# Performance work log

Measured on AMD Instinct MI355X. Metric: run time of the kernel, lower is better.

## Reference

```python
import jax, jax.numpy as jnp
import numpy as np

N = 50000
E = 1600000
D_IN = 128
D_HID = 64
BN_EPS = 1e-5


def setup_inputs() -> dict:
    key = jax.random.key(0)
    ks = jax.random.split(key, 12)
    x = jax.random.normal(ks[0], (N, D_IN), dtype=jnp.float32)
    edge_index_sc = jax.random.randint(ks[1], (2, E), 0, N, dtype=jnp.int64)
    edge_weight_sc = jax.random.uniform(ks[2], (E,), dtype=jnp.float32)
    edge_index_fc = jax.random.randint(ks[3], (2, E), 0, N, dtype=jnp.int64)
    edge_weight_fc = jax.random.uniform(ks[4], (E,), dtype=jnp.float32)
    # learned parameters
    alpha = jnp.float32(0.5)
    W1 = jax.random.normal(ks[5], (D_IN, D_HID), dtype=jnp.float32) / np.sqrt(D_IN)
    b1 = jnp.zeros((D_HID,), dtype=jnp.float32)
    W2 = jax.random.normal(ks[6], (D_HID, D_HID), dtype=jnp.float32) / np.sqrt(D_HID)
    b2 = jnp.zeros((D_HID,), dtype=jnp.float32)
    gamma1 = jnp.ones((D_HID,), dtype=jnp.float32)
    beta1 = jnp.zeros((D_HID,), dtype=jnp.float32)
    gamma2 = jnp.ones((D_HID,), dtype=jnp.float32)
    beta2 = jnp.zeros((D_HID,), dtype=jnp.float32)
    return {"x": x, "edge_index_sc": edge_index_sc, "edge_weight_sc": edge_weight_sc,
            "edge_index_fc": edge_index_fc, "edge_weight_fc": edge_weight_fc,
            "alpha": alpha, "W1": W1, "b1": b1, "W2": W2, "b2": b2,
            "gamma1": gamma1, "beta1": beta1, "gamma2": gamma2, "beta2": beta2}


def _gcn_layer(h, W, b, src, dst, norm, n):
    # h: [N, d_in] -> [N, d_out]; PyG GCNConv: transform, then weighted scatter-add
    h = h @ W
    msg = h[src] * norm[:, None]                # [E+N, d_out] gather + scale
    out = jax.ops.segment_sum(msg, dst, num_segments=n)
    return out + b


def _bn_relu(h, gamma, beta):
    # BatchNorm1d (training-mode batch stats, biased variance) + ReLU
    mean = jnp.mean(h, axis=0)
    var = jnp.var(h, axis=0)
    h = (h - mean) * jax.lax.rsqrt(var + BN_EPS) * gamma + beta
    return jax.nn.relu(h)


def reference(x, edge_index_sc, edge_weight_sc, edge_index_fc, edge_weight_fc,
              alpha, W1, b1, W2, b2, gamma1, beta1, gamma2, beta2):
    n = x.shape[0]
    a = jax.nn.sigmoid(alpha)
    # mixed weights on SC topology (edge_index_fc unused, as in original)
    w_mix = a * edge_weight_sc + (1.0 - a) * edge_weight_fc
    # add self loops (weight 1) and compute symmetric GCN normalization
    loop = jnp.arange(n, dtype=edge_index_sc.dtype)
    src = jnp.concatenate([edge_index_sc[0], loop])
    dst = jnp.concatenate([edge_index_sc[1], loop])
    w = jnp.concatenate([w_mix, jnp.ones((n,), dtype=w_mix.dtype)])
    deg = jax.ops.segment_sum(w, dst, num_segments=n)
    dinv = jnp.where(deg > 0, jax.lax.rsqrt(jnp.maximum(deg, 1e-12)), 0.0)
    norm = dinv[src] * w * dinv[dst]
    h = _gcn_layer(x, W1, b1, src, dst, norm, n)
    h = _bn_relu(h, gamma1, beta1)
    h = _gcn_layer(h, W2, b2, src, dst, norm, n)
    h = _bn_relu(h, gamma2, beta2)
    return h  # dropout is identity in eval mode
```

## Files before the change

### kernel.cpp

```cpp
#include <hip/hip_runtime.h>
#include <hip/hip_fp16.h>
#include <math.h>

#define N_NODES 50000
#define N_EDGES 1600000
#define D_INF   128
#define D_HID   64
#define BN_EPS  1e-5f
#define NBINS   391
#define BINCAP  4608
#define EPB     6250
#define GEMM1B  3125
#define NPAIR   3125
#define NCOPY   64

struct SmGemm { float sw[D_INF * D_HID]; float sx[16 * D_INF]; };
struct SmBin  { int hcnt[NBINS]; int hbase[NBINS]; };
union SmPre { SmGemm g; SmBin a; };

__global__ __launch_bounds__(256) void k_pre(const float* __restrict__ wsc,
                                             const float* __restrict__ wfc,
                                             const int*   __restrict__ ei,
                                             const float* __restrict__ alpha,
                                             int* __restrict__ bin_cur,
                                             unsigned long long* __restrict__ binned,
                                             const float* __restrict__ x,
                                             const float* __restrict__ W,
                                             __half* __restrict__ ha,
                                             __half* __restrict__ hb) {
    __shared__ SmPre sm;
    int t = threadIdx.x;
    if (blockIdx.x < 256) {
        int e0 = blockIdx.x * EPB;
        for (int b = t; b < NBINS; b += 256) sm.a.hcnt[b] = 0;
        __syncthreads();
        for (int i = t; i < EPB; i += 256)
            atomicAdd(&sm.a.hcnt[ei[N_EDGES + e0 + i] >> 7], 1);
        __syncthreads();
        for (int b = t; b < NBINS; b += 256) {
            int c = sm.a.hcnt[b];
            sm.a.hbase[b] = c ? atomicAdd(&bin_cur[b], c) : 0;
            sm.a.hcnt[b] = 0;
        }
        __syncthreads();
        float a = 1.0f / (1.0f + expf(-alpha[0]));
        for (int i = t; i < EPB; i += 256) {
            int e = e0 + i;
            int s = ei[e], d = ei[N_EDGES + e];
            float wm = fmaf(a, wsc[e] - wfc[e], wfc[e]);
            int bin = d >> 7;
            int slot = atomicAdd(&sm.a.hcnt[bin], 1);
            int gpos = sm.a.hbase[bin] + slot;
            if (gpos < BINCAP) {
                unsigned long long ent =
                    ((unsigned long long)__float_as_uint(wm) << 32)
                    | (unsigned int)(s | ((d & 127) << 16));
                binned[(size_t)bin * BINCAP + gpos] = ent;
            }
        }
    } else {
        int row0 = (blockIdx.x - 256) * 16;
#pragma unroll
        for (int j = 0; j < 32; ++j) sm.g.sw[t + j * 256] = W[t + j * 256];
#pragma unroll
        for (int j = 0; j < 8; ++j) {
            int i = t + j * 256;
            int r = i >> 7, k = i & 127;
            sm.g.sx[i] = x[(row0 + r) * D_INF + k];
        }
        __syncthreads();
        int c = t & 63, rg = (t >> 6) * 4;
        float a0 = 0, a1 = 0, a2 = 0, a3 = 0;
#pragma unroll 4
        for (int k = 0; k < D_INF; ++k) {
            float w = sm.g.sw[k * D_HID + c];
            a0 = fmaf(sm.g.sx[(rg + 0) * D_INF + k], w, a0);
            a1 = fmaf(sm.g.sx[(rg + 1) * D_INF + k], w, a1);
            a2 = fmaf(sm.g.sx[(rg + 2) * D_INF + k], w, a2);
            a3 = fmaf(sm.g.sx[(rg + 3) * D_INF + k], w, a3);
        }
        __half* tbl = (c < 32) ? ha : hb;
        int cc = c & 31;
        tbl[(row0 + rg + 0) * 32 + cc] = __float2half_rn(a0);
        tbl[(row0 + rg + 1) * 32 + cc] = __float2half_rn(a1);
        tbl[(row0 + rg + 2) * 32 + cc] = __float2half_rn(a2);
        tbl[(row0 + rg + 3) * 32 + cc] = __float2half_rn(a3);
    }
}

__global__ __launch_bounds__(512) void k_binB(const int* __restrict__ bin_cur,
                                              const unsigned long long* __restrict__ binned,
                                              int2*  __restrict__ row_se,
                                              float* __restrict__ dinv,
                                              __half* __restrict__ ha,
                                              __half* __restrict__ hb,
                                              unsigned int* __restrict__ csr) {
    __shared__ unsigned long long stage[BINCAP];
    __shared__ int   ncnt[128];
    __shared__ float ndeg[128];
    __shared__ int   sscan[128];
    __shared__ float sdinv[128];
    __shared__ int   lb[128];
    int t = threadIdx.x;
    int bin = blockIdx.x;
    if (t < 128) { ncnt[t] = 0; ndeg[t] = 0.0f; }
    int cnt = min(bin_cur[bin], BINCAP);
    const unsigned long long* mybin = binned + (size_t)bin * BINCAP;
    for (int i = t; i < cnt; i += 512) stage[i] = mybin[i];
    __syncthreads();
    for (int i = t; i < cnt; i += 512) {
        unsigned long long ent = stage[i];
        unsigned int lo = (unsigned int)ent;
        int nl = (lo >> 16) & 127;
        float wm = __uint_as_float((unsigned int)(ent >> 32));
        atomicAdd(&ncnt[nl], 1);
        atomicAdd(&ndeg[nl], wm);
    }
    __syncthreads();
    int node0 = bin << 7;
    int nnodes = min(128, N_NODES - node0);
    if (t < 128) {
        float dv = rsqrtf(1.0f + ndeg[t]);
        sdinv[t] = dv;
        if (t < nnodes) dinv[node0 + t] = dv;
        sscan[t] = ncnt[t];
    }
    __syncthreads();
    for (int off = 1; off < 128; off <<= 1) {
        int u = (t >= off && t < 128) ? sscan[t - off] : 0;
        __syncthreads();
        if (t < 128) sscan[t] += u;
        __syncthreads();
    }
    if (t < nnodes) {
        int s = bin * BINCAP + sscan[t] - ncnt[t];
        row_se[node0 + t] = make_int2(s, s + ncnt[t]);
        lb[t] = s;
    }
    __syncthreads();
    int nh = nnodes * 32;
    for (int i = t; i < nh; i += 512) {
        int n = i >> 5, c = i & 31;
        float dv = sdinv[n];
        int idx = (node0 + n) * 32 + c;
        ha[idx] = __float2half_rn(__half2float(ha[idx]) * dv);
        hb[idx] = __float2half_rn(__half2float(hb[idx]) * dv);
    }
    if (t < 128) ncnt[t] = 0;
    __syncthreads();
    for (int i = t; i < cnt; i += 512) {
        unsigned long long ent = stage[i];
        unsigned int lo = (unsigned int)ent;
        int nl  = (lo >> 16) & 127;
        int src = lo & 0xFFFFu;
        float wm = __uint_as_float((unsigned int)(ent >> 32));
        int slot = atomicAdd(&ncnt[nl], 1);
        unsigned short wh = __half_as_ushort(__float2half_rn(wm));
        csr[lb[nl] + slot] = (unsigned int)src | ((unsigned int)wh << 16);
    }
}

__device__ inline float hdec(unsigned int u) {
    return __half2float(__ushort_as_half((unsigned short)(u >> 16)));
}

__global__ __launch_bounds__(512) void k_gather(const __half* __restrict__ ha,
                                                const __half* __restrict__ hb,
                                                const unsigned int* __restrict__ csr,
                                                const int2*  __restrict__ row_se,
                                                const float* __restrict__ dinv,
                                                const float* __restrict__ bias,
                                                float* __restrict__ out,
                                                float* __restrict__ stat) {
    __shared__ float s1[512], s2[512];
    int t = threadIdx.x;
    int half = blockIdx.x & 1;
    const float4* __restrict__ h4 = (const float4*)(half ? hb : ha);
    int node = (blockIdx.x >> 1) * 16 + (t >> 5);
    int ln = t & 31;
    int sg = ln >> 2;
    int cq = ln & 3;
    int2 se = row_se[node];
    float dd = dinv[node];
    float acc[8];
    if (sg == 0) {
        float4 sv = h4[node * 4 + cq];
        const __half2* p = reinterpret_cast<const __half2*>(&sv);
#pragma unroll
        for (int i = 0; i < 4; ++i) {
            float2 f = __half22float2(p[i]);
            acc[2 * i] = f.x; acc[2 * i + 1] = f.y;
        }
    } else {
#pragma unroll
        for (int i = 0; i < 8; ++i) acc[i] = 0.0f;
    }
    for (int b = se.x; b < se.y; b += 32) {
        int c0 = min(32, se.y - b);
        int cm = c0 - 1;
        unsigned int my = (ln < c0) ? csr[b + ln] : 0u;
        unsigned int u0 = __shfl(my, min(sg,      cm), 32);
        unsigned int u1 = __shfl(my, min(sg + 8,  cm), 32);
        unsigned int u2 = __shfl(my, min(sg + 16, cm), 32);
        unsigned int u3 = __shfl(my, min(sg + 24, cm), 32);
        float4 r0 = h4[(u0 & 0xFFFFu) * 4 + cq];
        float4 r1 = h4[(u1 & 0xFFFFu) * 4 + cq];
        float4 r2 = h4[(u2 & 0xFFFFu) * 4 + cq];
        float4 r3 = h4[(u3 & 0xFFFFu) * 4 + cq];
        float w0 = (sg      < c0) ? hdec(u0) : 0.0f;
        float w1 = (sg + 8  < c0) ? hdec(u1) : 0.0f;
        float w2 = (sg + 16 < c0) ? hdec(u2) : 0.0f;
        float w3 = (sg + 24 < c0) ? hdec(u3) : 0.0f;
        const __half2* p0 = reinterpret_cast<const __half2*>(&r0);
        const __half2* p1 = reinterpret_cast<const __half2*>(&r1);
        const __half2* p2 = reinterpret_cast<const __half2*>(&r2);
        const __half2* p3 = reinterpret_cast<const __half2*>(&r3);
#pragma unroll
        for (int i = 0; i < 4; ++i) {
            float2 f0 = __half22float2(p0[i]);
            float2 f1 = __half22float2(p1[i]);
            float2 f2 = __half22float2(p2[i]);
            float2 f3 = __half22float2(p3[i]);
            acc[2*i]   = fmaf(f0.x, w0, acc[2*i]);
            acc[2*i+1] = fmaf(f0.y, w0, acc[2*i+1]);
            acc[2*i]   = fmaf(f1.x, w1, acc[2*i]);
            acc[2*i+1] = fmaf(f1.y, w1, acc[2*i+1]);
            acc[2*i]   = fmaf(f2.x, w2, acc[2*i]);
            acc[2*i+1] = fmaf(f2.y, w2, acc[2*i+1]);
            acc[2*i]   = fmaf(f3.x, w3, acc[2*i]);
            acc[2*i+1] = fmaf(f3.y, w3, acc[2*i+1]);
        }
    }
#pragma unroll
    for (int off = 16; off >= 4; off >>= 1) {
#pragma unroll
        for (int i = 0; i < 8; ++i) acc[i] += __shfl_down(acc[i], off, 32);
    }
    if (ln < 4) {
        int col0 = half * 32 + cq * 8;
        float v[8];
#pragma unroll
        for (int i = 0; i < 8; ++i) v[i] = fmaf(acc[i], dd, bias[col0 + i]);
        float4* o = (float4*)out;
        o[node * 16 + half * 8 + cq * 2]     = make_float4(v[0], v[1], v[2], v[3]);
        o[node * 16 + half * 8 + cq * 2 + 1] = make_float4(v[4], v[5], v[6], v[7]);
        int lb = (t >> 5) * 32 + cq * 8;
#pragma unroll
        for (int i = 0; i < 8; ++i) { s1[lb + i] = v[i]; s2[lb + i] = v[i] * v[i]; }
    }
    __syncthreads();
#pragma unroll
    for (int off = 256; off >= 32; off >>= 1) {
        if (t < off) { s1[t] += s1[t + off]; s2[t] += s2[t + off]; }
        __syncthreads();
    }
    if (t < 32) {
        int cp = (blockIdx.x >> 1) & (NCOPY - 1);
        int col = half * 32 + t;
        atomicAdd(&stat[cp * 128 + col],      s1[t]);
        atomicAdd(&stat[cp * 128 + 64 + col], s2[t]);
    }
}

__global__ __launch_bounds__(256) void k_gemm2_bn(const float* __restrict__ hin,
                                                  const float* __restrict__ stat,
                                                  const float* __restrict__ gamma,
                                                  const float* __restrict__ beta,
                                                  const float* __restrict__ W,
                                                  const float* __restrict__ dinv,
                                                  __half* __restrict__ ha,
                                                  __half* __restrict__ hb) {
    __shared__ float sw[D_HID * D_HID];
    __shared__ float sx[16 * D_HID];
    __shared__ float sc[D_HID], sh[D_HID];
    int t = threadIdx.x;
    int row0 = blockIdx.x * 16;
#pragma unroll
    for (int j = 0; j < 16; ++j) sw[t + j * 256] = W[t + j * 256];
    if (t < 64) {
        float s = 0.0f, q = 0.0f;
#pragma unroll 8
        for (int c = 0; c < NCOPY; ++c) {
            s += stat[c * 128 + t];
            q += stat[c * 128 + 64 + t];
        }
        const float invn = 1.0f / (float)N_NODES;
        float mean = s * invn;
        float var  = q * invn - mean * mean;
        float g    = gamma[t] * rsqrtf(var + BN_EPS);
        sc[t] = g;
        sh[t] = beta[t] - mean * g;
    }
    __syncthreads();
#pragma unroll
    for (int j = 0; j < 4; ++j) {
        int i = t + j * 256;
        int k = i & 63;
        sx[i] = fmaxf(0.0f, fmaf(hin[row0 * D_HID + i], sc[k], sh[k]));
    }
    __syncthreads();
    int c = t & 63, rg = (t >> 6) * 4;
    float a0 = 0, a1 = 0, a2 = 0, a3 = 0;
#pragma unroll 4
    for (int k = 0; k < D_HID; ++k) {
        float w = sw[k * D_HID + c];
        a0 = fmaf(sx[(rg + 0) * D_HID + k], w, a0);
        a1 = fmaf(sx[(rg + 1) * D_HID + k], w, a1);
        a2 = fmaf(sx[(rg + 2) * D_HID + k], w, a2);
        a3 = fmaf(sx[(rg + 3) * D_HID + k], w, a3);
    }
    __half* tbl = (c < 32) ? ha : hb;
    int cc = c & 31;
    tbl[(row0 + rg + 0) * 32 + cc] = __float2half_rn(a0 * dinv[row0 + rg + 0]);
    tbl[(row0 + rg + 1) * 32 + cc] = __float2half_rn(a1 * dinv[row0 + rg + 1]);
    tbl[(row0 + rg + 2) * 32 + cc] = __float2half_rn(a2 * dinv[row0 + rg + 2]);
    tbl[(row0 + rg + 3) * 32 + cc] = __float2half_rn(a3 * dinv[row0 + rg + 3]);
}

__global__ __launch_bounds__(256) void k_bn_apply_relu(float4* __restrict__ h,
                                                       const float* __restrict__ stat,
                                                       const float* __restrict__ gamma,
                                                       const float* __restrict__ beta) {
    __shared__ float sc[D_HID], sh[D_HID];
    int t = threadIdx.x;
    if (t < 64) {
        float s = 0.0f, q = 0.0f;
#pragma unroll 8
        for (int c = 0; c < NCOPY; ++c) {
            s += stat[c * 128 + t];
            q += stat[c * 128 + 64 + t];
        }
        const float invn = 1.0f / (float)N_NODES;
        float mean = s * invn;
        float var  = q * invn - mean * mean;
        float g    = gamma[t] * rsqrtf(var + BN_EPS);
        sc[t] = g;
        sh[t] = beta[t] - mean * g;
    }
    __syncthreads();
    int idx = blockIdx.x * 256 + t;
    if (idx >= N_NODES * D_HID / 4) return;
    int j = (idx & 15) * 4;
    float4 v = h[idx];
    v.x = fmaxf(0.0f, fmaf(v.x, sc[j],     sh[j]));
    v.y = fmaxf(0.0f, fmaf(v.y, sc[j + 1], sh[j + 1]));
    v.z = fmaxf(0.0f, fmaf(v.z, sc[j + 2], sh[j + 2]));
    v.w = fmaxf(0.0f, fmaf(v.w, sc[j + 3], sh[j + 3]));
    h[idx] = v;
}

extern "C" void kernel_launch(void* const* d_in, const int* in_sizes, int n_in,
                              void* d_out, int out_size, void* d_ws, size_t ws_size,
                              hipStream_t stream) {
    const float* x     = (const float*)d_in[0];
    const int*   ei_sc = (const int*)  d_in[1];
    const float* w_sc  = (const float*)d_in[2];
    const float* w_fc  = (const float*)d_in[4];
    const float* alpha = (const float*)d_in[5];
    const float* W1    = (const float*)d_in[6];
    const float* b1    = (const float*)d_in[7];
    const float* W2    = (const float*)d_in[8];
    const float* b2    = (const float*)d_in[9];
    const float* g1    = (const float*)d_in[10];
    const float* be1   = (const float*)d_in[11];
    const float* g2    = (const float*)d_in[12];
    const float* be2   = (const float*)d_in[13];
    float* out = (float*)d_out;

    unsigned long long* binned = (unsigned long long*)d_ws;
    int2*  row_se  = (int2*)(binned + (size_t)NBINS * BINCAP);
    int*   bin_cur = (int*)(row_se + N_NODES);
    float* stats   = (float*)(bin_cur + 400);
    float* dinv    = stats + 2 * NCOPY * 128;
    unsigned int* csr = (unsigned int*)(dinv + N_NODES);
    __half* ha     = (__half*)(csr + (size_t)NBINS * BINCAP);
    __half* hb     = ha + (size_t)N_NODES * 32;
    float* agg     = (float*)(hb + (size_t)N_NODES * 32);

    const int gV4 = (N_NODES * D_HID / 4 + 255) / 256;
    const int gGA = NPAIR * 2;
    const int gGM = N_NODES / 16;

    hipMemsetAsync(bin_cur, 0, (400 + 2 * NCOPY * 128) * sizeof(int), stream);
    k_pre <<<256 + GEMM1B, 256, 0, stream>>>(w_sc, w_fc, ei_sc, alpha,
                                             bin_cur, binned, x, W1, ha, hb);
    k_binB<<<NBINS, 512, 0, stream>>>(bin_cur, binned, row_se, dinv, ha, hb, csr);

    k_gather  <<<gGA, 512, 0, stream>>>(ha, hb, csr, row_se, dinv, b1, agg, stats);

    k_gemm2_bn<<<gGM, 256, 0, stream>>>(agg, stats, g1, be1, W2, dinv, ha, hb);
    k_gather  <<<gGA, 512, 0, stream>>>(ha, hb, csr, row_se, dinv, b2, out,
                                        stats + NCOPY * 128);
    k_bn_apply_relu<<<gV4, 256, 0, stream>>>((float4*)out, stats + NCOPY * 128,
                                             g2, be2);
}
```

Before: 284.8 us.

## Fuse post-binning stages into one persistent cooperative kernel with grid syncs

```diff
diff --git a/kernel.cpp b/kernel.cpp
--- a/kernel.cpp
+++ b/kernel.cpp
@@ -1,4 +1,5 @@
 #include <hip/hip_runtime.h>
+#include <hip/hip_cooperative_groups.h>
 #include <hip/hip_fp16.h>
 #include <math.h>
 
@@ -88,95 +89,91 @@
     }
 }
 
-__global__ __launch_bounds__(512) void k_binB(const int* __restrict__ bin_cur,
-                                              const unsigned long long* __restrict__ binned,
-                                              int2*  __restrict__ row_se,
-                                              float* __restrict__ dinv,
-                                              __half* __restrict__ ha,
-                                              __half* __restrict__ hb,
-                                              unsigned int* __restrict__ csr) {
-    __shared__ unsigned long long stage[BINCAP];
-    __shared__ int   ncnt[128];
-    __shared__ float ndeg[128];
-    __shared__ int   sscan[128];
-    __shared__ float sdinv[128];
-    __shared__ int   lb[128];
-    int t = threadIdx.x;
-    int bin = blockIdx.x;
-    if (t < 128) { ncnt[t] = 0; ndeg[t] = 0.0f; }
+struct SmBinB {
+    unsigned long long stage[BINCAP];
+    int   ncnt[128];
+    float ndeg[128];
+    int   sscan[128];
+    float sdinv[128];
+    int   lb[128];
+};
+struct SmGath { float s1[512]; float s2[512]; };
+struct SmG2   { float sw[D_HID * D_HID]; float sx[16 * D_HID];
+                float sc[D_HID]; float sh[D_HID]; };
+union SmMega { SmBinB b; SmGath s; SmG2 g; };
+
+__device__ __forceinline__ void binB_body(int bin, int t, SmBinB& s,
+        const int* bin_cur, const unsigned long long* binned,
+        int2* row_se, float* dinv, __half* ha, __half* hb, unsigned int* csr) {
+    if (t < 128) { s.ncnt[t] = 0; s.ndeg[t] = 0.0f; }
     int cnt = min(bin_cur[bin], BINCAP);
     const unsigned long long* mybin = binned + (size_t)bin * BINCAP;
-    for (int i = t; i < cnt; i += 512) stage[i] = mybin[i];
+    for (int i = t; i < cnt; i += 512) s.stage[i] = mybin[i];
     __syncthreads();
     for (int i = t; i < cnt; i += 512) {
-        unsigned long long ent = stage[i];
+        unsigned long long ent = s.stage[i];
         unsigned int lo = (unsigned int)ent;
         int nl = (lo >> 16) & 127;
         float wm = __uint_as_float((unsigned int)(ent >> 32));
-        atomicAdd(&ncnt[nl], 1);
-        atomicAdd(&ndeg[nl], wm);
+        atomicAdd(&s.ncnt[nl], 1);
+        atomicAdd(&s.ndeg[nl], wm);
     }
     __syncthreads();
     int node0 = bin << 7;
     int nnodes = min(128, N_NODES - node0);
     if (t < 128) {
-        float dv = rsqrtf(1.0f + ndeg[t]);
-        sdinv[t] = dv;
+        float dv = rsqrtf(1.0f + s.ndeg[t]);
+        s.sdinv[t] = dv;
         if (t < nnodes) dinv[node0 + t] = dv;
-        sscan[t] = ncnt[t];
+        s.sscan[t] = s.ncnt[t];
     }
     __syncthreads();
     for (int off = 1; off < 128; off <<= 1) {
-        int u = (t >= off && t < 128) ? sscan[t - off] : 0;
-        __syncthreads();
-        if (t < 128) sscan[t] += u;
+        int u = (t >= off && t < 128) ? s.sscan[t - off] : 0;
+        __syncthreads();
+        if (t < 128) s.sscan[t] += u;
         __syncthreads();
     }
     if (t < nnodes) {
-        int s = bin * BINCAP + sscan[t] - ncnt[t];
-        row_se[node0 + t] = make_int2(s, s + ncnt[t]);
-        lb[t] = s;
+        int st = bin * BINCAP + s.sscan[t] - s.ncnt[t];
+        row_se[node0 + t] = make_int2(st, st + s.ncnt[t]);
+        s.lb[t] = st;
     }
     __syncthreads();
     int nh = nnodes * 32;
     for (int i = t; i < nh; i += 512) {
         int n = i >> 5, c = i & 31;
-        float dv = sdinv[n];
+        float dv = s.sdinv[n];
         int idx = (node0 + n) * 32 + c;
         ha[idx] = __float2half_rn(__half2float(ha[idx]) * dv);
         hb[idx] = __float2half_rn(__half2float(hb[idx]) * dv);
     }
-    if (t < 128) ncnt[t] = 0;
+    if (t < 128) s.ncnt[t] = 0;
     __syncthreads();
     for (int i = t; i < cnt; i += 512) {
-        unsigned long long ent = stage[i];
+        unsigned long long ent = s.stage[i];
         unsigned int lo = (unsigned int)ent;
         int nl  = (lo >> 16) & 127;
         int src = lo & 0xFFFFu;
         float wm = __uint_as_float((unsigned int)(ent >> 32));
-        int slot = atomicAdd(&ncnt[nl], 1);
+        int slot = atomicAdd(&s.ncnt[nl], 1);
         unsigned short wh = __half_as_ushort(__float2half_rn(wm));
-        csr[lb[nl] + slot] = (unsigned int)src | ((unsigned int)wh << 16);
-    }
+        csr[s.lb[nl] + slot] = (unsigned int)src | ((unsigned int)wh << 16);
+    }
+    __syncthreads();
 }
 
 __device__ inline float hdec(unsigned int u) {
     return __half2float(__ushort_as_half((unsigned short)(u >> 16)));
 }
 
-__global__ __launch_bounds__(512) void k_gather(const __half* __restrict__ ha,
-                                                const __half* __restrict__ hb,
-                                                const unsigned int* __restrict__ csr,
-                                                const int2*  __restrict__ row_se,
-                                                const float* __restrict__ dinv,
-                                                const float* __restrict__ bias,
-                                                float* __restrict__ out,
-                                                float* __restrict__ stat) {
-    __shared__ float s1[512], s2[512];
-    int t = threadIdx.x;
-    int half = blockIdx.x & 1;
-    const float4* __restrict__ h4 = (const float4*)(half ? hb : ha);
-    int node = (blockIdx.x >> 1) * 16 + (t >> 5);
+__device__ __forceinline__ void gather_body(int vb, int t, SmGath& sm,
+        const __half* ha, const __half* hb, const unsigned int* csr,
+        const int2* row_se, const float* dinv, const float* bias,
+        float* out, float* stat) {
+    int half = vb & 1;
+    const float4* h4 = (const float4*)(half ? hb : ha);
+    int node = (vb >> 1) * 16 + (t >> 5);
     int ln = t & 31;
     int sg = ln >> 2;
     int cq = ln & 3;
@@ -246,37 +243,25 @@
         o[node * 16 + half * 8 + cq * 2 + 1] = make_float4(v[4], v[5], v[6], v[7]);
         int lb = (t >> 5) * 32 + cq * 8;
 #pragma unroll
-        for (int i = 0; i < 8; ++i) { s1[lb + i] = v[i]; s2[lb + i] = v[i] * v[i]; }
+        for (int i = 0; i < 8; ++i) { sm.s1[lb + i] = v[i]; sm.s2[lb + i] = v[i] * v[i]; }
     }
     __syncthreads();
 #pragma unroll
     for (int off = 256; off >= 32; off >>= 1) {
-        if (t < off) { s1[t] += s1[t + off]; s2[t] += s2[t + off]; }
+        if (t < off) { sm.s1[t] += sm.s1[t + off]; sm.s2[t] += sm.s2[t + off]; }
         __syncthreads();
     }
     if (t < 32) {
-        int cp = (blockIdx.x >> 1) & (NCOPY - 1);
+        int cp = (vb >> 1) & (NCOPY - 1);
         int col = half * 32 + t;
-        atomicAdd(&stat[cp * 128 + col],      s1[t]);
-        atomicAdd(&stat[cp * 128 + 64 + col], s2[t]);
-    }
-}
-
-__global__ __launch_bounds__(256) void k_gemm2_bn(const float* __restrict__ hin,
-                                                  const float* __restrict__ stat,
-                                                  const float* __restrict__ gamma,
-                                                  const float* __restrict__ beta,
-                                                  const float* __restrict__ W,
-                                                  const float* __restrict__ dinv,
-                                                  __half* __restrict__ ha,
-                                                  __half* __restrict__ hb) {
-    __shared__ float sw[D_HID * D_HID];
-    __shared__ float sx[16 * D_HID];
-    __shared__ float sc[D_HID], sh[D_HID];
-    int t = threadIdx.x;
-    int row0 = blockIdx.x * 16;
-#pragma unroll
-    for (int j = 0; j < 16; ++j) sw[t + j * 256] = W[t + j * 256];
+        atomicAdd(&stat[cp * 128 + col],      sm.s1[t]);
+        atomicAdd(&stat[cp * 128 + 64 + col], sm.s2[t]);
+    }
+    __syncthreads();
+}
+
+__device__ __forceinline__ void bn_coef(int t, float* sc, float* sh,
+        const float* stat, const float* gamma, const float* beta) {
     if (t < 64) {
         float s = 0.0f, q = 0.0f;
 #pragma unroll 8
@@ -291,62 +276,118 @@
         sc[t] = g;
         sh[t] = beta[t] - mean * g;
     }
-    __syncthreads();
-#pragma unroll
-    for (int j = 0; j < 4; ++j) {
-        int i = t + j * 256;
+}
+
+__device__ __forceinline__ void gemm2_sub(int row0, int t, SmG2& g,
+        const float* hin, const float* dinv, __half* ha, __half* hb) {
+#pragma unroll
+    for (int j = 0; j < 2; ++j) {
+        int i = t + j * 512;
         int k = i & 63;
-        sx[i] = fmaxf(0.0f, fmaf(hin[row0 * D_HID + i], sc[k], sh[k]));
-    }
-    __syncthreads();
-    int c = t & 63, rg = (t >> 6) * 4;
-    float a0 = 0, a1 = 0, a2 = 0, a3 = 0;
+        g.sx[i] = fmaxf(0.0f, fmaf(hin[row0 * D_HID + i], g.sc[k], g.sh[k]));
+    }
+    __syncthreads();
+    int c = t & 63, r2 = (t >> 6) * 2;
+    float a0 = 0, a1 = 0;
 #pragma unroll 4
     for (int k = 0; k < D_HID; ++k) {
-        float w = sw[k * D_HID + c];
-        a0 = fmaf(sx[(rg + 0) * D_HID + k], w, a0);
-        a1 = fmaf(sx[(rg + 1) * D_HID + k], w, a1);
-        a2 = fmaf(sx[(rg + 2) * D_HID + k], w, a2);
-        a3 = fmaf(sx[(rg + 3) * D_HID + k], w, a3);
+        float w = g.sw[k * D_HID + c];
+        a0 = fmaf(g.sx[(r2 + 0) * D_HID + k], w, a0);
+        a1 = fmaf(g.sx[(r2 + 1) * D_HID + k], w, a1);
     }
     __half* tbl = (c < 32) ? ha : hb;
     int cc = c & 31;
-    tbl[(row0 + rg + 0) * 32 + cc] = __float2half_rn(a0 * dinv[row0 + rg + 0]);
-    tbl[(row0 + rg + 1) * 32 + cc] = __float2half_rn(a1 * dinv[row0 + rg + 1]);
-    tbl[(row0 + rg + 2) * 32 + cc] = __float2half_rn(a2 * dinv[row0 + rg + 2]);
-    tbl[(row0 + rg + 3) * 32 + cc] = __float2half_rn(a3 * dinv[row0 + rg + 3]);
-}
-
-__global__ __launch_bounds__(256) void k_bn_apply_relu(float4* __restrict__ h,
-                                                       const float* __restrict__ stat,
-                                                       const float* __restrict__ gamma,
-                                                       const float* __restrict__ beta) {
+    tbl[(row0 + r2 + 0) * 32 + cc] = __float2half_rn(a0 * dinv[row0 + r2 + 0]);
+    tbl[(row0 + r2 + 1) * 32 + cc] = __float2half_rn(a1 * dinv[row0 + r2 + 1]);
+    __syncthreads();
+}
+
+__global__ __launch_bounds__(512, 6) void k_mega(
+        const int* bin_cur, const unsigned long long* binned,
+        int2* row_se, float* dinv, __half* ha, __half* hb, unsigned int* csr,
+        float* agg, float* stats, const float* b1,
+        const float* g1, const float* be1, const float* W2,
+        const float* b2, float* out, const float* g2, const float* be2) {
+    __shared__ SmMega sm;
+    int t = threadIdx.x;
+    int nb = gridDim.x;
+    cooperative_groups::grid_group gg = cooperative_groups::this_grid();
+
+    for (int i = blockIdx.x * 512 + t; i < 2 * NCOPY * 128; i += nb * 512)
+        stats[i] = 0.0f;
+    for (int bin = blockIdx.x; bin < NBINS; bin += nb)
+        binB_body(bin, t, sm.b, bin_cur, binned, row_se, dinv, ha, hb, csr);
+    gg.sync();
+
+    for (int vb = blockIdx.x; vb < NPAIR * 2; vb += nb)
+        gather_body(vb, t, sm.s, ha, hb, csr, row_se, dinv, b1, agg, stats);
+    gg.sync();
+
+    bn_coef(t, sm.g.sc, sm.g.sh, stats, g1, be1);
+#pragma unroll
+    for (int j = 0; j < 8; ++j) sm.g.sw[t + j * 512] = W2[t + j * 512];
+    __syncthreads();
+    for (int vb = blockIdx.x; vb < N_NODES / 16; vb += nb)
+        gemm2_sub(vb * 16, t, sm.g, agg, dinv, ha, hb);
+    gg.sync();
+
+    for (int vb = blockIdx.x; vb < NPAIR * 2; vb += nb)
+        gather_body(vb, t, sm.s, ha, hb, csr, row_se, dinv, b2, out,
+                    stats + NCOPY * 128);
+    gg.sync();
+
+    bn_coef(t, sm.g.sc, sm.g.sh, stats + NCOPY * 128, g2, be2);
+    __syncthreads();
+    float4* o4 = (float4*)out;
+    for (int i = blockIdx.x * 512 + t; i < N_NODES * 16; i += nb * 512) {
+        int j = (i & 15) * 4;
+        float4 v = o4[i];
+        v.x = fmaxf(0.0f, fmaf(v.x, sm.g.sc[j],     sm.g.sh[j]));
+        v.y = fmaxf(0.0f, fmaf(v.y, sm.g.sc[j + 1], sm.g.sh[j + 1]));
+        v.z = fmaxf(0.0f, fmaf(v.z, sm.g.sc[j + 2], sm.g.sh[j + 2]));
+        v.w = fmaxf(0.0f, fmaf(v.w, sm.g.sc[j + 3], sm.g.sh[j + 3]));
+        o4[i] = v;
+    }
+}
+
+__global__ __launch_bounds__(512) void k_binB_w(const int* bin_cur,
+        const unsigned long long* binned, int2* row_se, float* dinv,
+        __half* ha, __half* hb, unsigned int* csr) {
+    __shared__ SmBinB s;
+    binB_body(blockIdx.x, threadIdx.x, s, bin_cur, binned, row_se, dinv, ha, hb, csr);
+}
+__global__ __launch_bounds__(512) void k_gath_w(const __half* ha, const __half* hb,
+        const unsigned int* csr, const int2* row_se, const float* dinv,
+        const float* bias, float* out, float* stat) {
+    __shared__ SmGath s;
+    gather_body(blockIdx.x, threadIdx.x, s, ha, hb, csr, row_se, dinv, bias, out, stat);
+}
+__global__ __launch_bounds__(512) void k_g2_w(const float* hin, const float* stat,
+        const float* gamma, const float* beta, const float* W,
+        const float* dinv, __half* ha, __half* hb) {
+    __shared__ SmG2 g;
+    int t = threadIdx.x;
+    bn_coef(t, g.sc, g.sh, stat, gamma, beta);
+#pragma unroll
+    for (int j = 0; j < 8; ++j) g.sw[t + j * 512] = W[t + j * 512];
+    __syncthreads();
+    gemm2_sub(blockIdx.x * 16, t, g, hin, dinv, ha, hb);
+}
+__global__ __launch_bounds__(512) void k_bnap_w(float4* h, const float* stat,
+        const float* gamma, const float* beta) {
     __shared__ float sc[D_HID], sh[D_HID];
     int t = threadIdx.x;
-    if (t < 64) {
-        float s = 0.0f, q = 0.0f;
-#pragma unroll 8
-        for (int c = 0; c < NCOPY; ++c) {
-            s += stat[c * 128 + t];
-            q += stat[c * 128 + 64 + t];
-        }
-        const float invn = 1.0f / (float)N_NODES;
-        float mean = s * invn;
-        float var  = q * invn - mean * mean;
-        float g    = gamma[t] * rsqrtf(var + BN_EPS);
-        sc[t] = g;
-        sh[t] = beta[t] - mean * g;
-    }
-    __syncthreads();
-    int idx = blockIdx.x * 256 + t;
-    if (idx >= N_NODES * D_HID / 4) return;
-    int j = (idx & 15) * 4;
-    float4 v = h[idx];
-    v.x = fmaxf(0.0f, fmaf(v.x, sc[j],     sh[j]));
-    v.y = fmaxf(0.0f, fmaf(v.y, sc[j + 1], sh[j + 1]));
-    v.z = fmaxf(0.0f, fmaf(v.z, sc[j + 2], sh[j + 2]));
-    v.w = fmaxf(0.0f, fmaf(v.w, sc[j + 3], sh[j + 3]));
-    h[idx] = v;
+    bn_coef(t, sc, sh, stat, gamma, beta);
+    __syncthreads();
+    for (int i = blockIdx.x * 512 + t; i < N_NODES * 16; i += gridDim.x * 512) {
+        int j = (i & 15) * 4;
+        float4 v = h[i];
+        v.x = fmaxf(0.0f, fmaf(v.x, sc[j],     sh[j]));
+        v.y = fmaxf(0.0f, fmaf(v.y, sc[j + 1], sh[j + 1]));
+        v.z = fmaxf(0.0f, fmaf(v.z, sc[j + 2], sh[j + 2]));
+        v.w = fmaxf(0.0f, fmaf(v.w, sc[j + 3], sh[j + 3]));
+        h[i] = v;
+    }
 }
 
 extern "C" void kernel_launch(void* const* d_in, const int* in_sizes, int n_in,
@@ -377,20 +418,44 @@
     __half* hb     = ha + (size_t)N_NODES * 32;
     float* agg     = (float*)(hb + (size_t)N_NODES * 32);
 
-    const int gV4 = (N_NODES * D_HID / 4 + 255) / 256;
-    const int gGA = NPAIR * 2;
-    const int gGM = N_NODES / 16;
-
     hipMemsetAsync(bin_cur, 0, (400 + 2 * NCOPY * 128) * sizeof(int), stream);
-    k_pre <<<256 + GEMM1B, 256, 0, stream>>>(w_sc, w_fc, ei_sc, alpha,
-                                             bin_cur, binned, x, W1, ha, hb);
-    k_binB<<<NBINS, 512, 0, stream>>>(bin_cur, binned, row_se, dinv, ha, hb, csr);
-
-    k_gather  <<<gGA, 512, 0, stream>>>(ha, hb, csr, row_se, dinv, b1, agg, stats);
-
-    k_gemm2_bn<<<gGM, 256, 0, stream>>>(agg, stats, g1, be1, W2, dinv, ha, hb);
-    k_gather  <<<gGA, 512, 0, stream>>>(ha, hb, csr, row_se, dinv, b2, out,
-                                        stats + NCOPY * 128);
-    k_bn_apply_relu<<<gV4, 256, 0, stream>>>((float4*)out, stats + NCOPY * 128,
-                                             g2, be2);
-}
+    k_pre<<<256 + GEMM1B, 256, 0, stream>>>(w_sc, w_fc, ei_sc, alpha,
+                                            bin_cur, binned, x, W1, ha, hb);
+
+    static int bpc = 0;
+    if (bpc == 0) {
+        int v = 0;
+        if (hipOccupancyMaxActiveBlocksPerMultiprocessor(&v, k_mega, 512, 0)
+                == hipSuccess && v > 0) bpc = v;
+        else bpc = 2;
+        if (bpc > 4) bpc = 4;
+    }
+    int nb = bpc * 256;
+
+    const int*   a_bc = bin_cur;  const unsigned long long* a_bn = binned;
+    int2*  a_rs = row_se;  float* a_dv = dinv;
+    __half* a_ha = ha;     __half* a_hb = hb;   unsigned int* a_cs = csr;
+    float* a_ag = agg;     float* a_st = stats;
+    const float* a_b1 = b1, *a_g1 = g1, *a_e1 = be1, *a_w2 = W2;
+    const float* a_b2 = b2, *a_g2 = g2, *a_e2 = be2;
+    float* a_ou = out;
+    void* margs[] = { (void*)&a_bc, (void*)&a_bn, (void*)&a_rs, (void*)&a_dv,
+                      (void*)&a_ha, (void*)&a_hb, (void*)&a_cs, (void*)&a_ag,
+                      (void*)&a_st, (void*)&a_b1, (void*)&a_g1, (void*)&a_e1,
+                      (void*)&a_w2, (void*)&a_b2, (void*)&a_ou, (void*)&a_g2,
+                      (void*)&a_e2 };
+    hipError_t ce = hipLaunchCooperativeKernel((const void*)k_mega, dim3(nb),
+                                               dim3(512), margs, 0, stream);
+    if (ce != hipSuccess) {
+        k_binB_w<<<NBINS, 512, 0, stream>>>(bin_cur, binned, row_se, dinv,
+                                            ha, hb, csr);
+        k_gath_w<<<NPAIR * 2, 512, 0, stream>>>(ha, hb, csr, row_se, dinv,
+                                                b1, agg, stats);
+        k_g2_w  <<<N_NODES / 16, 512, 0, stream>>>(agg, stats, g1, be1, W2,
+                                                   dinv, ha, hb);
+        k_gath_w<<<NPAIR * 2, 512, 0, stream>>>(ha, hb, csr, row_se, dinv,
+                                                b2, out, stats + NCOPY * 128);
+        k_bnap_w<<<1563, 512, 0, stream>>>((float4*)out, stats + NCOPY * 128,
+                                           g2, be2);
+    }
+}
```

Measured after the change: 537.6 us. 1.89x slower.

## Fuse CSR build with first gather and fold source dinv into edge weights

Applied to the files above, without the earlier changes.

```diff
diff --git a/kernel.cpp b/kernel.cpp
--- a/kernel.cpp
+++ b/kernel.cpp
@@ -24,6 +24,7 @@
                                              const float* __restrict__ alpha,
                                              int* __restrict__ bin_cur,
                                              unsigned long long* __restrict__ binned,
+                                             float* __restrict__ deg,
                                              const float* __restrict__ x,
                                              const float* __restrict__ W,
                                              __half* __restrict__ ha,
@@ -48,6 +49,7 @@
             int e = e0 + i;
             int s = ei[e], d = ei[N_EDGES + e];
             float wm = fmaf(a, wsc[e] - wfc[e], wfc[e]);
+            atomicAdd(&deg[d], wm);
             int bin = d >> 7;
             int slot = atomicAdd(&sm.a.hcnt[bin], 1);
             int gpos = sm.a.hbase[bin] + slot;
@@ -88,80 +90,183 @@
     }
 }
 
-__global__ __launch_bounds__(512) void k_binB(const int* __restrict__ bin_cur,
-                                              const unsigned long long* __restrict__ binned,
-                                              int2*  __restrict__ row_se,
-                                              float* __restrict__ dinv,
-                                              __half* __restrict__ ha,
-                                              __half* __restrict__ hb,
-                                              unsigned int* __restrict__ csr) {
-    __shared__ unsigned long long stage[BINCAP];
+__device__ inline float hdec(unsigned int u) {
+    return __half2float(__ushort_as_half((unsigned short)(u >> 16)));
+}
+
+__global__ __launch_bounds__(512) void k_fused(const int* __restrict__ bin_cur,
+                                               const unsigned long long* __restrict__ binned,
+                                               const float* __restrict__ deg,
+                                               int2*  __restrict__ row_se,
+                                               float* __restrict__ dinv,
+                                               const __half* __restrict__ ha,
+                                               const __half* __restrict__ hb,
+                                               unsigned int* __restrict__ csr,
+                                               const float* __restrict__ bias,
+                                               float* __restrict__ out,
+                                               float* __restrict__ stat) {
+    __shared__ union {
+        unsigned long long stage[BINCAP];
+        struct { float s1[512]; float s2[512]; } r;
+    } u;
+    __shared__ unsigned int csr_l[BINCAP];
     __shared__ int   ncnt[128];
-    __shared__ float ndeg[128];
     __shared__ int   sscan[128];
+    __shared__ int   lbl[128];
     __shared__ float sdinv[128];
-    __shared__ int   lb[128];
     int t = threadIdx.x;
     int bin = blockIdx.x;
-    if (t < 128) { ncnt[t] = 0; ndeg[t] = 0.0f; }
-    int cnt = min(bin_cur[bin], BINCAP);
-    const unsigned long long* mybin = binned + (size_t)bin * BINCAP;
-    for (int i = t; i < cnt; i += 512) stage[i] = mybin[i];
-    __syncthreads();
-    for (int i = t; i < cnt; i += 512) {
-        unsigned long long ent = stage[i];
-        unsigned int lo = (unsigned int)ent;
-        int nl = (lo >> 16) & 127;
-        float wm = __uint_as_float((unsigned int)(ent >> 32));
-        atomicAdd(&ncnt[nl], 1);
-        atomicAdd(&ndeg[nl], wm);
-    }
-    __syncthreads();
     int node0 = bin << 7;
     int nnodes = min(128, N_NODES - node0);
+    if (t < 128) ncnt[t] = 0;
+    int cntb = min(bin_cur[bin], BINCAP);
+    const unsigned long long* mybin = binned + (size_t)bin * BINCAP;
+    for (int i = t; i < cntb; i += 512) u.stage[i] = mybin[i];
+    __syncthreads();
+    for (int i = t; i < cntb; i += 512)
+        atomicAdd(&ncnt[((unsigned int)u.stage[i] >> 16) & 127], 1);
+    __syncthreads();
     if (t < 128) {
-        float dv = rsqrtf(1.0f + ndeg[t]);
+        float dv = rsqrtf(1.0f + ((t < nnodes) ? deg[node0 + t] : 0.0f));
         sdinv[t] = dv;
         if (t < nnodes) dinv[node0 + t] = dv;
         sscan[t] = ncnt[t];
     }
     __syncthreads();
     for (int off = 1; off < 128; off <<= 1) {
-        int u = (t >= off && t < 128) ? sscan[t - off] : 0;
-        __syncthreads();
-        if (t < 128) sscan[t] += u;
-        __syncthreads();
-    }
-    if (t < nnodes) {
-        int s = bin * BINCAP + sscan[t] - ncnt[t];
-        row_se[node0 + t] = make_int2(s, s + ncnt[t]);
-        lb[t] = s;
-    }
-    __syncthreads();
-    int nh = nnodes * 32;
-    for (int i = t; i < nh; i += 512) {
-        int n = i >> 5, c = i & 31;
-        float dv = sdinv[n];
-        int idx = (node0 + n) * 32 + c;
-        ha[idx] = __float2half_rn(__half2float(ha[idx]) * dv);
-        hb[idx] = __float2half_rn(__half2float(hb[idx]) * dv);
-    }
+        int v2 = (t >= off && t < 128) ? sscan[t - off] : 0;
+        __syncthreads();
+        if (t < 128) sscan[t] += v2;
+        __syncthreads();
+    }
+    if (t < 128) {
+        int lb = sscan[t] - ncnt[t];
+        lbl[t] = lb;
+        if (t < nnodes) {
+            int g0 = bin * BINCAP + lb;
+            row_se[node0 + t] = make_int2(g0, g0 + ncnt[t]);
+        }
+    }
+    __syncthreads();
     if (t < 128) ncnt[t] = 0;
     __syncthreads();
-    for (int i = t; i < cnt; i += 512) {
-        unsigned long long ent = stage[i];
+    unsigned int* gcsr = csr + (size_t)bin * BINCAP;
+    for (int i = t; i < cntb; i += 512) {
+        unsigned long long ent = u.stage[i];
         unsigned int lo = (unsigned int)ent;
         int nl  = (lo >> 16) & 127;
         int src = lo & 0xFFFFu;
         float wm = __uint_as_float((unsigned int)(ent >> 32));
+        float ds = rsqrtf(1.0f + deg[src]);
         int slot = atomicAdd(&ncnt[nl], 1);
-        unsigned short wh = __half_as_ushort(__float2half_rn(wm));
-        csr[lb[nl] + slot] = (unsigned int)src | ((unsigned int)wh << 16);
-    }
-}
-
-__device__ inline float hdec(unsigned int u) {
-    return __half2float(__ushort_as_half((unsigned short)(u >> 16)));
+        int pos = lbl[nl] + slot;
+        unsigned short wh = __half_as_ushort(__float2half_rn(wm * ds));
+        unsigned int w = (unsigned int)src | ((unsigned int)wh << 16);
+        csr_l[pos] = w;
+        gcsr[pos] = w;
+    }
+    __syncthreads();
+    int g  = t >> 5;
+    int ln = t & 31;
+    int sg = ln >> 2, cq = ln & 3;
+    int h  = g & 1;
+    const float4* __restrict__ h4 = (const float4*)(h ? hb : ha);
+    float accS[8], accQ[8];
+#pragma unroll
+    for (int i = 0; i < 8; ++i) { accS[i] = 0.0f; accQ[i] = 0.0f; }
+    int nvh = nnodes * 2;
+    for (int vh = g; vh < nvh; vh += 16) {
+        int nloc = vh >> 1;
+        int node = node0 + nloc;
+        float dd = sdinv[nloc];
+        int s0 = lbl[nloc];
+        int s1e = s0 + ncnt[nloc];
+        float acc[8];
+        if (sg == 0) {
+            float4 sv = h4[node * 4 + cq];
+            const __half2* p = reinterpret_cast<const __half2*>(&sv);
+#pragma unroll
+            for (int i = 0; i < 4; ++i) {
+                float2 f = __half22float2(p[i]);
+                acc[2 * i] = f.x * dd; acc[2 * i + 1] = f.y * dd;
+            }
+        } else {
+#pragma unroll
+            for (int i = 0; i < 8; ++i) acc[i] = 0.0f;
+        }
+        for (int b = s0; b < s1e; b += 32) {
+            int c0 = min(32, s1e - b);
+            int cm = c0 - 1;
+            unsigned int u0 = csr_l[b + min(sg,      cm)];
+            unsigned int u1 = csr_l[b + min(sg + 8,  cm)];
+            unsigned int u2 = csr_l[b + min(sg + 16, cm)];
+            unsigned int u3 = csr_l[b + min(sg + 24, cm)];
+            float4 r0 = h4[(u0 & 0xFFFFu) * 4 + cq];
+            float4 r1 = h4[(u1 & 0xFFFFu) * 4 + cq];
+            float4 r2 = h4[(u2 & 0xFFFFu) * 4 + cq];
+            float4 r3 = h4[(u3 & 0xFFFFu) * 4 + cq];
+            float w0 = (sg      < c0) ? hdec(u0) : 0.0f;
+            float w1 = (sg + 8  < c0) ? hdec(u1) : 0.0f;
+            float w2 = (sg + 16 < c0) ? hdec(u2) : 0.0f;
+            float w3 = (sg + 24 < c0) ? hdec(u3) : 0.0f;
+            const __half2* p0 = reinterpret_cast<const __half2*>(&r0);
+            const __half2* p1 = reinterpret_cast<const __half2*>(&r1);
+            const __half2* p2 = reinterpret_cast<const __half2*>(&r2);
+            const __half2* p3 = reinterpret_cast<const __half2*>(&r3);
+#pragma unroll
+            for (int i = 0; i < 4; ++i) {
+                float2 f0 = __half22float2(p0[i]);
+                float2 f1 = __half22float2(p1[i]);
+                float2 f2 = __half22float2(p2[i]);
+                float2 f3 = __half22float2(p3[i]);
+                acc[2*i]   = fmaf(f0.x, w0, acc[2*i]);
+                acc[2*i+1] = fmaf(f0.y, w0, acc[2*i+1]);
+                acc[2*i]   = fmaf(f1.x, w1, acc[2*i]);
+                acc[2*i+1] = fmaf(f1.y, w1, acc[2*i+1]);
+                acc[2*i]   = fmaf(f2.x, w2, acc[2*i]);
+                acc[2*i+1] = fmaf(f2.y, w2, acc[2*i+1]);
+                acc[2*i]   = fmaf(f3.x, w3, acc[2*i]);
+                acc[2*i+1] = fmaf(f3.y, w3, acc[2*i+1]);
+            }
+        }
+#pragma unroll
+        for (int off = 16; off >= 4; off >>= 1) {
+#pragma unroll
+            for (int i = 0; i < 8; ++i) acc[i] += __shfl_down(acc[i], off, 32);
+        }
+        if (ln < 4) {
+            int col0 = h * 32 + cq * 8;
+            float v[8];
+#pragma unroll
+            for (int i = 0; i < 8; ++i) v[i] = fmaf(acc[i], dd, bias[col0 + i]);
+            float4* o = (float4*)out;
+            o[node * 16 + h * 8 + cq * 2]     = make_float4(v[0], v[1], v[2], v[3]);
+            o[node * 16 + h * 8 + cq * 2 + 1] = make_float4(v[4], v[5], v[6], v[7]);
+#pragma unroll
+            for (int i = 0; i < 8; ++i) { accS[i] += v[i]; accQ[i] += v[i] * v[i]; }
+        }
+    }
+    __syncthreads();
+    if (ln < 4) {
+#pragma unroll
+        for (int i = 0; i < 8; ++i) {
+            u.r.s1[g * 32 + cq * 8 + i] = accS[i];
+            u.r.s2[g * 32 + cq * 8 + i] = accQ[i];
+        }
+    }
+    __syncthreads();
+    if (t < 64) {
+        int hh = t >> 5, c32 = t & 31;
+        float s = 0.0f, q = 0.0f;
+#pragma unroll
+        for (int k = 0; k < 8; ++k) {
+            s += u.r.s1[(2 * k + hh) * 32 + c32];
+            q += u.r.s2[(2 * k + hh) * 32 + c32];
+        }
+        int cp = bin & (NCOPY - 1);
+        atomicAdd(&stat[cp * 128 + t],      s);
+        atomicAdd(&stat[cp * 128 + 64 + t], q);
+    }
 }
 
 __global__ __launch_bounds__(512) void k_gather(const __half* __restrict__ ha,
@@ -189,7 +294,7 @@
 #pragma unroll
         for (int i = 0; i < 4; ++i) {
             float2 f = __half22float2(p[i]);
-            acc[2 * i] = f.x; acc[2 * i + 1] = f.y;
+            acc[2 * i] = f.x * dd; acc[2 * i + 1] = f.y * dd;
         }
     } else {
 #pragma unroll
@@ -267,7 +372,6 @@
                                                   const float* __restrict__ gamma,
                                                   const float* __restrict__ beta,
                                                   const float* __restrict__ W,
-                                                  const float* __restrict__ dinv,
                                                   __half* __restrict__ ha,
                                                   __half* __restrict__ hb) {
     __shared__ float sw[D_HID * D_HID];
@@ -311,10 +415,10 @@
     }
     __half* tbl = (c < 32) ? ha : hb;
     int cc = c & 31;
-    tbl[(row0 + rg + 0) * 32 + cc] = __float2half_rn(a0 * dinv[row0 + rg + 0]);
-    tbl[(row0 + rg + 1) * 32 + cc] = __float2half_rn(a1 * dinv[row0 + rg + 1]);
-    tbl[(row0 + rg + 2) * 32 + cc] = __float2half_rn(a2 * dinv[row0 + rg + 2]);
-    tbl[(row0 + rg + 3) * 32 + cc] = __float2half_rn(a3 * dinv[row0 + rg + 3]);
+    tbl[(row0 + rg + 0) * 32 + cc] = __float2half_rn(a0);
+    tbl[(row0 + rg + 1) * 32 + cc] = __float2half_rn(a1);
+    tbl[(row0 + rg + 2) * 32 + cc] = __float2half_rn(a2);
+    tbl[(row0 + rg + 3) * 32 + cc] = __float2half_rn(a3);
 }
 
 __global__ __launch_bounds__(256) void k_bn_apply_relu(float4* __restrict__ h,
@@ -371,7 +475,8 @@
     int2*  row_se  = (int2*)(binned + (size_t)NBINS * BINCAP);
     int*   bin_cur = (int*)(row_se + N_NODES);
     float* stats   = (float*)(bin_cur + 400);
-    float* dinv    = stats + 2 * NCOPY * 128;
+    float* deg     = stats + 2 * NCOPY * 128;
+    float* dinv    = deg + N_NODES;
     unsigned int* csr = (unsigned int*)(dinv + N_NODES);
     __half* ha     = (__half*)(csr + (size_t)NBINS * BINCAP);
     __half* hb     = ha + (size_t)N_NODES * 32;
@@ -381,14 +486,13 @@
     const int gGA = NPAIR * 2;
     const int gGM = N_NODES / 16;
 
-    hipMemsetAsync(bin_cur, 0, (400 + 2 * NCOPY * 128) * sizeof(int), stream);
-    k_pre <<<256 + GEMM1B, 256, 0, stream>>>(w_sc, w_fc, ei_sc, alpha,
-                                             bin_cur, binned, x, W1, ha, hb);
-    k_binB<<<NBINS, 512, 0, stream>>>(bin_cur, binned, row_se, dinv, ha, hb, csr);
-
-    k_gather  <<<gGA, 512, 0, stream>>>(ha, hb, csr, row_se, dinv, b1, agg, stats);
-
-    k_gemm2_bn<<<gGM, 256, 0, stream>>>(agg, stats, g1, be1, W2, dinv, ha, hb);
+    hipMemsetAsync(bin_cur, 0, (400 + 2 * NCOPY * 128 + N_NODES) * sizeof(int),
+                   stream);
+    k_pre  <<<256 + GEMM1B, 256, 0, stream>>>(w_sc, w_fc, ei_sc, alpha,
+                                              bin_cur, binned, deg, x, W1, ha, hb);
+    k_fused<<<NBINS, 512, 0, stream>>>(bin_cur, binned, deg, row_se, dinv,
+                                       ha, hb, csr, b1, agg, stats);
+    k_gemm2_bn<<<gGM, 256, 0, stream>>>(agg, stats, g1, be1, W2, ha, hb);
     k_gather  <<<gGA, 512, 0, stream>>>(ha, hb, csr, row_se, dinv, b2, out,
                                         stats + NCOPY * 128);
     k_bn_apply_relu<<<gV4, 256, 0, stream>>>((float4*)out, stats + NCOPY * 128,
```

Measured after the change: 336.2 us. 18.0% more time.
